# Kernel tuning notes

Hardware: AMD Instinct MI355X
Metric: run time of the kernel (lower is better)

The kernel has to match this reference:

```python
import jax, jax.numpy as jnp
import numpy as np

EMBED_DIM = 1024
NUM_HEADS = 16
HEAD_DIM = EMBED_DIM // NUM_HEADS


def setup_inputs() -> dict:
    key = jax.random.key(0)
    ks = jax.random.split(key, 6)
    s = 1.0 / np.sqrt(EMBED_DIM)
    x = jax.random.normal(ks[0], (2, 2048, EMBED_DIM), dtype=jnp.float32)
    # torch Linear weights are [out, in]; y = x @ W.T
    Wq = jax.random.uniform(ks[1], (EMBED_DIM, EMBED_DIM), jnp.float32, -s, s)
    Wk = jax.random.uniform(ks[2], (EMBED_DIM, EMBED_DIM), jnp.float32, -s, s)
    Wv = jax.random.uniform(ks[3], (EMBED_DIM, EMBED_DIM), jnp.float32, -s, s)
    Wo = jax.random.uniform(ks[4], (EMBED_DIM, EMBED_DIM), jnp.float32, -s, s)
    bo = jax.random.uniform(ks[5], (EMBED_DIM,), jnp.float32, -s, s)
    return {"x": x, "Wq": Wq, "Wk": Wk, "Wv": Wv, "Wo": Wo, "bo": bo}


def reference(x, Wq, Wk, Wv, Wo, bo):
    B, T, C = x.shape
    H, D = NUM_HEADS, HEAD_DIM
    # projections (torch Linear: x @ W.T)
    Q = (x @ Wq.T).reshape(B, T, H, D).transpose(0, 2, 1, 3)  # [B,H,T,D]
    K = (x @ Wk.T).reshape(B, T, H, D).transpose(0, 2, 1, 3)
    V = (x @ Wv.T).reshape(B, T, H, D).transpose(0, 2, 1, 3)
    scores = jnp.einsum('bhqd,bhkd->bhqk', Q, K) / jnp.sqrt(jnp.float32(D))
    causal = jnp.tril(jnp.ones((T, T), dtype=bool))
    scores = jnp.where(causal, scores, -jnp.inf)
    weights = jax.nn.softmax(scores, axis=-1)  # dropout=0.0 (eval): identity
    out = jnp.einsum('bhqk,bhkd->bhqd', weights, V)
    out = out.transpose(0, 2, 1, 3).reshape(B, T, C)
    return out @ Wo.T + bo
```

## Files before the change

### kernel.cpp

```cpp
#include <hip/hip_runtime.h>
#include <stdint.h>

typedef unsigned short u16;
typedef __bf16 bf16x4 __attribute__((ext_vector_type(4)));
typedef __bf16 bf16x8 __attribute__((ext_vector_type(8)));
typedef float f32x4 __attribute__((ext_vector_type(4)));

#define EMBED 1024
#define NHEAD 16
#define HDIM  64
#define BATCH 2
#define SEQ   2048
#define MROWS 4096

__device__ __forceinline__ u16 f2bf(float f) {
  union { float f; uint32_t u; } v; v.f = f;
  uint32_t u = v.u;
  return (u16)((u + 0x7FFFu + ((u >> 16) & 1u)) >> 16);
}

__device__ __forceinline__ float exp2_fast(float x) {
  float r; asm("v_exp_f32 %0, %1" : "=v"(r) : "v"(x)); return r;
}

__device__ __forceinline__ void gload16(const void* g, void* l) {
  __builtin_amdgcn_global_load_lds(
      (__attribute__((address_space(1))) uint32_t*)g,
      (__attribute__((address_space(3))) uint32_t*)l, 16, 0, 0);
}

__global__ __launch_bounds__(256) void convert_all(
    const float* __restrict__ x,  const float* __restrict__ wq,
    const float* __restrict__ wk, const float* __restrict__ wv,
    const float* __restrict__ wo,
    u16* __restrict__ xb, u16* __restrict__ wqb, u16* __restrict__ wkb,
    u16* __restrict__ wvb, u16* __restrict__ wob)
{
  int i4 = (blockIdx.x * 256 + threadIdx.x) * 4;
  const float* src; u16* dst; int off;
  if      (i4 < 4194304) { src = x;  dst = xb;  off = i4; }
  else if (i4 < 5242880) { src = wq; dst = wqb; off = i4 - 4194304; }
  else if (i4 < 6291456) { src = wk; dst = wkb; off = i4 - 5242880; }
  else if (i4 < 7340032) { src = wv; dst = wvb; off = i4 - 6291456; }
  else                   { src = wo; dst = wob; off = i4 - 7340032; }
  float4 v = *(const float4*)&src[off];
  ushort4 u;
  u.x = f2bf(v.x); u.y = f2bf(v.y); u.z = f2bf(v.z); u.w = f2bf(v.w);
  *(ushort4*)&dst[off] = u;
}

__global__ __launch_bounds__(256) void gemm_qkv(
    const u16* __restrict__ Ab, const u16* __restrict__ Wq,
    const u16* __restrict__ Wk, const u16* __restrict__ Wv,
    u16* __restrict__ Qb, u16* __restrict__ Kb, u16* __restrict__ Vt)
{
  const int bid = blockIdx.x;
  const int wg = (bid & 7) * 96 + (bid >> 3);
  const int my = wg / 24, nx = wg % 24;
  const int mode = nx >> 3;
  const u16* Bw = (mode == 0) ? Wq : (mode == 1) ? Wk : Wv;
  const int m0 = my * 128, n0 = (nx & 7) * 128;

  __shared__ __align__(16) u16 As[2][128 * 32];
  __shared__ __align__(16) u16 Bs[2][128 * 32];
  const int tid = threadIdx.x;
  const int lane = tid & 63, wid = tid >> 6;
  const int c = lane & 15, g = lane >> 4;
  const int wm = wid >> 1, wn = wid & 1;

  f32x4 acc[4][4] = {};

  auto stage = [&](int buf, int kt) {
#pragma unroll
    for (int i = 0; i < 2; ++i) {
      int ch = tid + i * 256;
      int row = ch >> 2, col8 = (ch & 3) * 8;
      gload16(Ab + (m0 + row) * 1024 + kt * 32 + col8, &As[buf][ch * 8]);
      gload16(Bw + (n0 + row) * 1024 + kt * 32 + col8, &Bs[buf][ch * 8]);
    }
  };

  stage(0, 0);
  __syncthreads();

  for (int kt = 0; kt < 32; ++kt) {
    const int cur = kt & 1;
    if (kt < 31) stage(cur ^ 1, kt + 1);
    bf16x8 af[4], bfr[4];
#pragma unroll
    for (int mi = 0; mi < 4; ++mi)
      af[mi] = *(const bf16x8*)&As[cur][(wm * 64 + mi * 16 + c) * 32 + g * 8];
#pragma unroll
    for (int ni = 0; ni < 4; ++ni)
      bfr[ni] = *(const bf16x8*)&Bs[cur][(wn * 64 + ni * 16 + c) * 32 + g * 8];
#pragma unroll
    for (int mi = 0; mi < 4; ++mi)
#pragma unroll
      for (int ni = 0; ni < 4; ++ni)
        acc[mi][ni] = __builtin_amdgcn_mfma_f32_16x16x32_bf16(
            af[mi], bfr[ni], acc[mi][ni], 0, 0, 0);
    __syncthreads();
  }

  const int gm = m0 + wm * 64;
  const int gn = n0 + wn * 64;
  if (mode < 2) {
    u16* Out = (mode == 0) ? Qb : Kb;
    const float sc = (mode == 0) ? 0.18033688011112042f : 1.0f;
#pragma unroll
    for (int mi = 0; mi < 4; ++mi)
#pragma unroll
      for (int ni = 0; ni < 4; ++ni)
#pragma unroll
        for (int r = 0; r < 4; ++r) {
          int m = gm + mi * 16 + 4 * g + r;
          int n = gn + ni * 16 + c;
          int b = m >> 11, t = m & 2047, h = n >> 6, d = n & 63;
          Out[((b * NHEAD + h) * SEQ + t) * HDIM + d] = f2bf(acc[mi][ni][r] * sc);
        }
  } else {
#pragma unroll
    for (int mi = 0; mi < 4; ++mi)
#pragma unroll
      for (int ni = 0; ni < 4; ++ni) {
        int m = gm + mi * 16 + 4 * g;
        int n = gn + ni * 16 + c;
        int b = m >> 11, t = m & 2047, h = n >> 6, d = n & 63;
        int tl = t & 63;
        int tp = (t & ~63) + (tl >> 5) * 32 + ((tl >> 2) & 3) * 8
                 + ((tl >> 4) & 1) * 4;
        ushort4 pk;
        pk.x = f2bf(acc[mi][ni][0]);
        pk.y = f2bf(acc[mi][ni][1]);
        pk.z = f2bf(acc[mi][ni][2]);
        pk.w = f2bf(acc[mi][ni][3]);
        *(ushort4*)&Vt[((b * NHEAD + h) * HDIM + d) * SEQ + tp] = pk;
      }
  }
}

__global__ __launch_bounds__(256, 4) void attn(
    const u16* __restrict__ Qb, const u16* __restrict__ Kb,
    const u16* __restrict__ Vt, u16* __restrict__ Ob)
{
  const int bid = blockIdx.x;
  const int xcd = bid & 7, d = bid >> 3;
  const int p = d >> 5, s = d & 31;
  const int bh = xcd * 4 + p;
  const int sp = (s + (p >> 1) * 16) & 31;
  const int qt = (p & 1) ? sp : 31 - sp;
  const int b = bh >> 4, h = bh & 15;
  const int q0 = qt * 64;

  __shared__ __align__(16) u16 Ks[2][64 * 64];
  __shared__ __align__(16) u16 Vs[2][64 * 64];

  const int tid = threadIdx.x, lane = tid & 63, w = tid >> 6;
  const int c = lane & 15, g = lane >> 4;

  const u16* Qg = Qb + bh * SEQ * HDIM;
  const u16* Kg = Kb + bh * SEQ * HDIM;
  const u16* Vg = Vt + bh * HDIM * SEQ;

  bf16x8 qf[2];
#pragma unroll
  for (int kk = 0; kk < 2; ++kk)
    qf[kk] = *(const bf16x8*)&Qg[(q0 + w * 16 + c) * HDIM + kk * 32 + g * 8];

  f32x4 o[4] = {};
  float lacc = 0.f;

  auto stage = [&](int buf, int j) {
    const int k0 = j * 64;
#pragma unroll
    for (int i = 0; i < 2; ++i) {
      int ch = tid + i * 256;
      int row = ch >> 3, c8 = ch & 7;
      int sc8 = c8 ^ (row & 7);
      gload16(Kg + (k0 + row) * HDIM + sc8 * 8, &Ks[buf][ch * 8]);
      gload16(Vg + row * SEQ + k0 + sc8 * 8, &Vs[buf][ch * 8]);
    }
  };

  stage(0, 0);
  __syncthreads();

  for (int j = 0; j <= qt; ++j) {
    const int cur = j & 1;
    if (j < qt) stage(cur ^ 1, j + 1);
    const int k0 = j * 64;

    f32x4 st[4] = {};
    __builtin_amdgcn_s_setprio(1);
#pragma unroll
    for (int kk = 0; kk < 2; ++kk)
#pragma unroll
      for (int kvt = 0; kvt < 4; ++kvt) {
        const int R = kvt * 16 + c;
        bf16x8 kf = *(const bf16x8*)
            &Ks[cur][R * 64 + (((kk * 4 + g) ^ (R & 7)) * 8)];
        st[kvt] = __builtin_amdgcn_mfma_f32_16x16x32_bf16(kf, qf[kk], st[kvt], 0, 0, 0);
      }
    __builtin_amdgcn_s_setprio(0);

    if (j == qt) {
      const int qrow = q0 + w * 16 + c;
#pragma unroll
      for (int kvt = 0; kvt < 4; ++kvt)
#pragma unroll
        for (int r = 0; r < 4; ++r) {
          int kv = k0 + kvt * 16 + 4 * g + r;
          st[kvt][r] = (kv <= qrow) ? st[kvt][r] : -1e30f;
        }
    }

    bf16x8 pa[2];
#pragma unroll
    for (int kvt = 0; kvt < 4; ++kvt)
#pragma unroll
      for (int r = 0; r < 4; ++r) {
        float p2 = exp2_fast(st[kvt][r]);
        lacc += p2;
        pa[kvt >> 1][(kvt & 1) * 4 + r] = (__bf16)p2;
      }

    __builtin_amdgcn_s_setprio(1);
#pragma unroll
    for (int kk = 0; kk < 2; ++kk)
#pragma unroll
      for (int ni = 0; ni < 4; ++ni) {
        const int dd = ni * 16 + c;
        bf16x8 vf = *(const bf16x8*)
            &Vs[cur][dd * 64 + (((kk * 4 + g) ^ (dd & 7)) * 8)];
        o[ni] = __builtin_amdgcn_mfma_f32_16x16x32_bf16(pa[kk], vf, o[ni], 0, 0, 0);
      }
    __builtin_amdgcn_s_setprio(0);

    __syncthreads();
  }

  float rs = lacc;
  rs += __shfl_xor(rs, 16);
  rs += __shfl_xor(rs, 32);
  const float inv = 1.0f / rs;
  float lr[4];
#pragma unroll
  for (int r = 0; r < 4; ++r) lr[r] = __shfl(inv, 4 * g + r);
#pragma unroll
  for (int ni = 0; ni < 4; ++ni)
#pragma unroll
    for (int r = 0; r < 4; ++r) {
      int nc = h * HDIM + ni * 16 + c;
      int mr = b * SEQ + q0 + w * 16 + 4 * g + r;
      Ob[mr * EMBED + nc] = f2bf(o[ni][r] * lr[r]);
    }
}

__global__ __launch_bounds__(256) void gemm_out(
    const u16* __restrict__ Ab, const u16* __restrict__ Bw,
    const float* __restrict__ bias, float* __restrict__ Out)
{
  const int bid = blockIdx.x;
  const int wg = (bid & 7) * 32 + (bid >> 3);
  const int my = wg >> 3, nx = wg & 7;
  const int m0 = my * 128, n0 = nx * 128;

  __shared__ __align__(16) u16 As[2][128 * 32];
  __shared__ __align__(16) u16 Bs[2][128 * 32];
  const int tid = threadIdx.x;
  const int lane = tid & 63, wid = tid >> 6;
  const int c = lane & 15, g = lane >> 4;
  const int wm = wid >> 1, wn = wid & 1;

  f32x4 acc[4][4] = {};

  auto stage = [&](int buf, int kt) {
#pragma unroll
    for (int i = 0; i < 2; ++i) {
      int ch = tid + i * 256;
      int row = ch >> 2, col8 = (ch & 3) * 8;
      gload16(Ab + (m0 + row) * 1024 + kt * 32 + col8, &As[buf][ch * 8]);
      gload16(Bw + (n0 + row) * 1024 + kt * 32 + col8, &Bs[buf][ch * 8]);
    }
  };

  stage(0, 0);
  __syncthreads();

  for (int kt = 0; kt < 32; ++kt) {
    const int cur = kt & 1;
    if (kt < 31) stage(cur ^ 1, kt + 1);
    bf16x8 af[4], bfr[4];
#pragma unroll
    for (int mi = 0; mi < 4; ++mi)
      af[mi] = *(const bf16x8*)&As[cur][(wm * 64 + mi * 16 + c) * 32 + g * 8];
#pragma unroll
    for (int ni = 0; ni < 4; ++ni)
      bfr[ni] = *(const bf16x8*)&Bs[cur][(wn * 64 + ni * 16 + c) * 32 + g * 8];
#pragma unroll
    for (int mi = 0; mi < 4; ++mi)
#pragma unroll
      for (int ni = 0; ni < 4; ++ni)
        acc[mi][ni] = __builtin_amdgcn_mfma_f32_16x16x32_bf16(
            af[mi], bfr[ni], acc[mi][ni], 0, 0, 0);
    __syncthreads();
  }

  const int gm = m0 + wm * 64;
  const int gn = n0 + wn * 64;
#pragma unroll
  for (int mi = 0; mi < 4; ++mi)
#pragma unroll
    for (int ni = 0; ni < 4; ++ni)
#pragma unroll
      for (int r = 0; r < 4; ++r) {
        int m = gm + mi * 16 + 4 * g + r;
        int n = gn + ni * 16 + c;
        Out[m * 1024 + n] = acc[mi][ni][r] + bias[n];
      }
}

extern "C" void kernel_launch(void* const* d_in, const int* in_sizes, int n_in,
                              void* d_out, int out_size, void* d_ws, size_t ws_size,
                              hipStream_t stream) {
  const float* x  = (const float*)d_in[0];
  const float* Wq = (const float*)d_in[1];
  const float* Wk = (const float*)d_in[2];
  const float* Wv = (const float*)d_in[3];
  const float* Wo = (const float*)d_in[4];
  const float* bo = (const float*)d_in[5];
  char* ws = (char*)d_ws;
  u16* xb  = (u16*)(ws);
  u16* wqb = (u16*)(ws + 8388608);
  u16* wkb = (u16*)(ws + 10485760);
  u16* wvb = (u16*)(ws + 12582912);
  u16* wob = (u16*)(ws + 14680064);
  u16* Qb  = (u16*)(ws + 16777216);
  u16* Kb  = (u16*)(ws + 25165824);
  u16* Vt  = (u16*)(ws + 33554432);
  u16* Ob  = (u16*)(ws + 41943040);

  convert_all<<<8192, 256, 0, stream>>>(x, Wq, Wk, Wv, Wo,
                                        xb, wqb, wkb, wvb, wob);
  gemm_qkv<<<dim3(768), 256, 0, stream>>>(xb, wqb, wkb, wvb, Qb, Kb, Vt);
  attn<<<dim3(1024), 256, 0, stream>>>(Qb, Kb, Vt, Ob);
  gemm_out<<<dim3(256), 256, 0, stream>>>(Ob, wob, bo, (float*)d_out);
}
```

Before: 111.4 us.

## Triple-buffer GEMM LDS staging with a single barrier per k-step

Result: slower. 128.6 us (+15.4%).

```diff
diff --git a/kernel.cpp b/kernel.cpp
--- a/kernel.cpp
+++ b/kernel.cpp
@@ -61,8 +61,8 @@
   const u16* Bw = (mode == 0) ? Wq : (mode == 1) ? Wk : Wv;
   const int m0 = my * 128, n0 = (nx & 7) * 128;
 
-  __shared__ __align__(16) u16 As[2][128 * 32];
-  __shared__ __align__(16) u16 Bs[2][128 * 32];
+  __shared__ __align__(16) u16 As[3][128 * 32];
+  __shared__ __align__(16) u16 Bs[3][128 * 32];
   const int tid = threadIdx.x;
   const int lane = tid & 63, wid = tid >> 6;
   const int c = lane & 15, g = lane >> 4;
@@ -80,27 +80,36 @@
     }
   };
 
-  stage(0, 0);
-  __syncthreads();
-
-  for (int kt = 0; kt < 32; ++kt) {
-    const int cur = kt & 1;
-    if (kt < 31) stage(cur ^ 1, kt + 1);
+  auto compute = [&](int buf) {
     bf16x8 af[4], bfr[4];
 #pragma unroll
     for (int mi = 0; mi < 4; ++mi)
-      af[mi] = *(const bf16x8*)&As[cur][(wm * 64 + mi * 16 + c) * 32 + g * 8];
+      af[mi] = *(const bf16x8*)&As[buf][(wm * 64 + mi * 16 + c) * 32 + g * 8];
 #pragma unroll
     for (int ni = 0; ni < 4; ++ni)
-      bfr[ni] = *(const bf16x8*)&Bs[cur][(wn * 64 + ni * 16 + c) * 32 + g * 8];
+      bfr[ni] = *(const bf16x8*)&Bs[buf][(wn * 64 + ni * 16 + c) * 32 + g * 8];
 #pragma unroll
     for (int mi = 0; mi < 4; ++mi)
 #pragma unroll
       for (int ni = 0; ni < 4; ++ni)
         acc[mi][ni] = __builtin_amdgcn_mfma_f32_16x16x32_bf16(
             af[mi], bfr[ni], acc[mi][ni], 0, 0, 0);
-    __syncthreads();
+  };
+
+  stage(0, 0);
+  stage(1, 1);
+  int cur = 0, nx2 = 2;
+  for (int kt = 0; kt < 31; ++kt) {
+    asm volatile("s_waitcnt vmcnt(4)" ::: "memory");
+    __builtin_amdgcn_s_barrier();
+    if (kt + 2 < 32) stage(nx2, kt + 2);
+    compute(cur);
+    cur = (cur == 2) ? 0 : cur + 1;
+    nx2 = (nx2 == 2) ? 0 : nx2 + 1;
   }
+  asm volatile("s_waitcnt vmcnt(0)" ::: "memory");
+  __builtin_amdgcn_s_barrier();
+  compute(cur);
 
   const int gm = m0 + wm * 64;
   const int gn = n0 + wn * 64;
@@ -265,8 +274,8 @@
   const int my = wg >> 3, nx = wg & 7;
   const int m0 = my * 128, n0 = nx * 128;
 
-  __shared__ __align__(16) u16 As[2][128 * 32];
-  __shared__ __align__(16) u16 Bs[2][128 * 32];
+  __shared__ __align__(16) u16 As[3][128 * 32];
+  __shared__ __align__(16) u16 Bs[3][128 * 32];
   const int tid = threadIdx.x;
   const int lane = tid & 63, wid = tid >> 6;
   const int c = lane & 15, g = lane >> 4;
@@ -284,27 +293,36 @@
     }
   };
 
-  stage(0, 0);
-  __syncthreads();
-
-  for (int kt = 0; kt < 32; ++kt) {
-    const int cur = kt & 1;
-    if (kt < 31) stage(cur ^ 1, kt + 1);
+  auto compute = [&](int buf) {
     bf16x8 af[4], bfr[4];
 #pragma unroll
     for (int mi = 0; mi < 4; ++mi)
-      af[mi] = *(const bf16x8*)&As[cur][(wm * 64 + mi * 16 + c) * 32 + g * 8];
+      af[mi] = *(const bf16x8*)&As[buf][(wm * 64 + mi * 16 + c) * 32 + g * 8];
 #pragma unroll
     for (int ni = 0; ni < 4; ++ni)
-      bfr[ni] = *(const bf16x8*)&Bs[cur][(wn * 64 + ni * 16 + c) * 32 + g * 8];
+      bfr[ni] = *(const bf16x8*)&Bs[buf][(wn * 64 + ni * 16 + c) * 32 + g * 8];
 #pragma unroll
     for (int mi = 0; mi < 4; ++mi)
 #pragma unroll
       for (int ni = 0; ni < 4; ++ni)
         acc[mi][ni] = __builtin_amdgcn_mfma_f32_16x16x32_bf16(
             af[mi], bfr[ni], acc[mi][ni], 0, 0, 0);
-    __syncthreads();
+  };
+
+  stage(0, 0);
+  stage(1, 1);
+  int cur = 0, nx2 = 2;
+  for (int kt = 0; kt < 31; ++kt) {
+    asm volatile("s_waitcnt vmcnt(4)" ::: "memory");
+    __builtin_amdgcn_s_barrier();
+    if (kt + 2 < 32) stage(nx2, kt + 2);
+    compute(cur);
+    cur = (cur == 2) ? 0 : cur + 1;
+    nx2 = (nx2 == 2) ? 0 : nx2 + 1;
   }
+  asm volatile("s_waitcnt vmcnt(0)" ::: "memory");
+  __builtin_amdgcn_s_barrier();
+  compute(cur);
 
   const int gm = m0 + wm * 64;
   const int gn = n0 + wn * 64;
```

## Pair complementary causal query tiles per attention block to balance work and share K/V

Applied to the files above, without the earlier changes.

Result: slower. 113.8 us (+2.1%).

```diff
diff --git a/kernel.cpp b/kernel.cpp
--- a/kernel.cpp
+++ b/kernel.cpp
@@ -139,18 +139,19 @@
   }
 }
 
-__global__ __launch_bounds__(256, 4) void attn(
+__global__ __launch_bounds__(256, 2) void attn(
     const u16* __restrict__ Qb, const u16* __restrict__ Kb,
     const u16* __restrict__ Vt, u16* __restrict__ Ob)
 {
   const int bid = blockIdx.x;
   const int xcd = bid & 7, d = bid >> 3;
-  const int p = d >> 5, s = d & 31;
-  const int bh = xcd * 4 + p;
-  const int sp = (s + (p >> 1) * 16) & 31;
-  const int qt = (p & 1) ? sp : 31 - sp;
+  const int cu = d & 31, half = d >> 5;
+  const int bh = xcd * 4 + (cu >> 3);
+  const int sp = cu & 7;
+  const int s = half ? (15 - sp) : sp;
+  const int qtA = s, qtB = 31 - s;
   const int b = bh >> 4, h = bh & 15;
-  const int q0 = qt * 64;
+  const int q0A = qtA * 64, q0B = qtB * 64;
 
   __shared__ __align__(16) u16 Ks[2][64 * 64];
   __shared__ __align__(16) u16 Vs[2][64 * 64];
@@ -162,13 +163,15 @@
   const u16* Kg = Kb + bh * SEQ * HDIM;
   const u16* Vg = Vt + bh * HDIM * SEQ;
 
-  bf16x8 qf[2];
-#pragma unroll
-  for (int kk = 0; kk < 2; ++kk)
-    qf[kk] = *(const bf16x8*)&Qg[(q0 + w * 16 + c) * HDIM + kk * 32 + g * 8];
-
-  f32x4 o[4] = {};
-  float lacc = 0.f;
+  bf16x8 qfA[2], qfB[2];
+#pragma unroll
+  for (int kk = 0; kk < 2; ++kk) {
+    qfA[kk] = *(const bf16x8*)&Qg[(q0A + w * 16 + c) * HDIM + kk * 32 + g * 8];
+    qfB[kk] = *(const bf16x8*)&Qg[(q0B + w * 16 + c) * HDIM + kk * 32 + g * 8];
+  }
+
+  f32x4 oA[4] = {}, oB[4] = {};
+  float laccA = 0.f, laccB = 0.f;
 
   auto stage = [&](int buf, int j) {
     const int k0 = j * 64;
@@ -185,74 +188,126 @@
   stage(0, 0);
   __syncthreads();
 
-  for (int j = 0; j <= qt; ++j) {
+  for (int j = 0; j <= qtB; ++j) {
     const int cur = j & 1;
-    if (j < qt) stage(cur ^ 1, j + 1);
+    if (j < qtB) stage(cur ^ 1, j + 1);
+    const bool dual = (j <= qtA);
     const int k0 = j * 64;
 
-    f32x4 st[4] = {};
+    f32x4 stA[4] = {}, stB[4] = {};
     __builtin_amdgcn_s_setprio(1);
-#pragma unroll
-    for (int kk = 0; kk < 2; ++kk)
-#pragma unroll
-      for (int kvt = 0; kvt < 4; ++kvt) {
-        const int R = kvt * 16 + c;
-        bf16x8 kf = *(const bf16x8*)
-            &Ks[cur][R * 64 + (((kk * 4 + g) ^ (R & 7)) * 8)];
-        st[kvt] = __builtin_amdgcn_mfma_f32_16x16x32_bf16(kf, qf[kk], st[kvt], 0, 0, 0);
-      }
+    if (dual) {
+#pragma unroll
+      for (int kk = 0; kk < 2; ++kk)
+#pragma unroll
+        for (int kvt = 0; kvt < 4; ++kvt) {
+          const int R = kvt * 16 + c;
+          bf16x8 kf = *(const bf16x8*)
+              &Ks[cur][R * 64 + (((kk * 4 + g) ^ (R & 7)) * 8)];
+          stB[kvt] = __builtin_amdgcn_mfma_f32_16x16x32_bf16(kf, qfB[kk], stB[kvt], 0, 0, 0);
+          stA[kvt] = __builtin_amdgcn_mfma_f32_16x16x32_bf16(kf, qfA[kk], stA[kvt], 0, 0, 0);
+        }
+    } else {
+#pragma unroll
+      for (int kk = 0; kk < 2; ++kk)
+#pragma unroll
+        for (int kvt = 0; kvt < 4; ++kvt) {
+          const int R = kvt * 16 + c;
+          bf16x8 kf = *(const bf16x8*)
+              &Ks[cur][R * 64 + (((kk * 4 + g) ^ (R & 7)) * 8)];
+          stB[kvt] = __builtin_amdgcn_mfma_f32_16x16x32_bf16(kf, qfB[kk], stB[kvt], 0, 0, 0);
+        }
+    }
     __builtin_amdgcn_s_setprio(0);
 
-    if (j == qt) {
-      const int qrow = q0 + w * 16 + c;
+    if (j == qtA) {
+      const int qrow = q0A + w * 16 + c;
 #pragma unroll
       for (int kvt = 0; kvt < 4; ++kvt)
 #pragma unroll
         for (int r = 0; r < 4; ++r) {
           int kv = k0 + kvt * 16 + 4 * g + r;
-          st[kvt][r] = (kv <= qrow) ? st[kvt][r] : -1e30f;
-        }
-    }
-
-    bf16x8 pa[2];
+          stA[kvt][r] = (kv <= qrow) ? stA[kvt][r] : -1e30f;
+        }
+    }
+    if (j == qtB) {
+      const int qrow = q0B + w * 16 + c;
+#pragma unroll
+      for (int kvt = 0; kvt < 4; ++kvt)
+#pragma unroll
+        for (int r = 0; r < 4; ++r) {
+          int kv = k0 + kvt * 16 + 4 * g + r;
+          stB[kvt][r] = (kv <= qrow) ? stB[kvt][r] : -1e30f;
+        }
+    }
+
+    bf16x8 paA[2], paB[2];
 #pragma unroll
     for (int kvt = 0; kvt < 4; ++kvt)
 #pragma unroll
       for (int r = 0; r < 4; ++r) {
-        float p2 = exp2_fast(st[kvt][r]);
-        lacc += p2;
-        pa[kvt >> 1][(kvt & 1) * 4 + r] = (__bf16)p2;
+        float pB = exp2_fast(stB[kvt][r]);
+        laccB += pB;
+        paB[kvt >> 1][(kvt & 1) * 4 + r] = (__bf16)pB;
       }
+    if (dual) {
+#pragma unroll
+      for (int kvt = 0; kvt < 4; ++kvt)
+#pragma unroll
+        for (int r = 0; r < 4; ++r) {
+          float pA = exp2_fast(stA[kvt][r]);
+          laccA += pA;
+          paA[kvt >> 1][(kvt & 1) * 4 + r] = (__bf16)pA;
+        }
+    }
 
     __builtin_amdgcn_s_setprio(1);
-#pragma unroll
-    for (int kk = 0; kk < 2; ++kk)
-#pragma unroll
-      for (int ni = 0; ni < 4; ++ni) {
-        const int dd = ni * 16 + c;
-        bf16x8 vf = *(const bf16x8*)
-            &Vs[cur][dd * 64 + (((kk * 4 + g) ^ (dd & 7)) * 8)];
-        o[ni] = __builtin_amdgcn_mfma_f32_16x16x32_bf16(pa[kk], vf, o[ni], 0, 0, 0);
-      }
+    if (dual) {
+#pragma unroll
+      for (int kk = 0; kk < 2; ++kk)
+#pragma unroll
+        for (int ni = 0; ni < 4; ++ni) {
+          const int dd = ni * 16 + c;
+          bf16x8 vf = *(const bf16x8*)
+              &Vs[cur][dd * 64 + (((kk * 4 + g) ^ (dd & 7)) * 8)];
+          oB[ni] = __builtin_amdgcn_mfma_f32_16x16x32_bf16(paB[kk], vf, oB[ni], 0, 0, 0);
+          oA[ni] = __builtin_amdgcn_mfma_f32_16x16x32_bf16(paA[kk], vf, oA[ni], 0, 0, 0);
+        }
+    } else {
+#pragma unroll
+      for (int kk = 0; kk < 2; ++kk)
+#pragma unroll
+        for (int ni = 0; ni < 4; ++ni) {
+          const int dd = ni * 16 + c;
+          bf16x8 vf = *(const bf16x8*)
+              &Vs[cur][dd * 64 + (((kk * 4 + g) ^ (dd & 7)) * 8)];
+          oB[ni] = __builtin_amdgcn_mfma_f32_16x16x32_bf16(paB[kk], vf, oB[ni], 0, 0, 0);
+        }
+    }
     __builtin_amdgcn_s_setprio(0);
 
     __syncthreads();
   }
 
-  float rs = lacc;
-  rs += __shfl_xor(rs, 16);
-  rs += __shfl_xor(rs, 32);
-  const float inv = 1.0f / rs;
-  float lr[4];
-#pragma unroll
-  for (int r = 0; r < 4; ++r) lr[r] = __shfl(inv, 4 * g + r);
+  float rsA = laccA, rsB = laccB;
+  rsA += __shfl_xor(rsA, 16); rsA += __shfl_xor(rsA, 32);
+  rsB += __shfl_xor(rsB, 16); rsB += __shfl_xor(rsB, 32);
+  const float invA = 1.0f / rsA, invB = 1.0f / rsB;
+  float lrA[4], lrB[4];
+#pragma unroll
+  for (int r = 0; r < 4; ++r) {
+    lrA[r] = __shfl(invA, 4 * g + r);
+    lrB[r] = __shfl(invB, 4 * g + r);
+  }
 #pragma unroll
   for (int ni = 0; ni < 4; ++ni)
 #pragma unroll
     for (int r = 0; r < 4; ++r) {
       int nc = h * HDIM + ni * 16 + c;
-      int mr = b * SEQ + q0 + w * 16 + 4 * g + r;
-      Ob[mr * EMBED + nc] = f2bf(o[ni][r] * lr[r]);
+      int mrA = b * SEQ + q0A + w * 16 + 4 * g + r;
+      Ob[mrA * EMBED + nc] = f2bf(oA[ni][r] * lrA[r]);
+      int mrB = b * SEQ + q0B + w * 16 + 4 * g + r;
+      Ob[mrB * EMBED + nc] = f2bf(oB[ni][r] * lrB[r]);
     }
 }
 
@@ -343,6 +398,6 @@
   convert_all<<<8192, 256, 0, stream>>>(x, Wq, Wk, Wv, Wo,
                                         xb, wqb, wkb, wvb, wob);
   gemm_qkv<<<dim3(768), 256, 0, stream>>>(xb, wqb, wkb, wvb, Qb, Kb, Vt);
-  attn<<<dim3(1024), 256, 0, stream>>>(Qb, Kb, Vt, Ob);
+  attn<<<dim3(512), 256, 0, stream>>>(Qb, Kb, Vt, Ob);
   gemm_out<<<dim3(256), 256, 0, stream>>>(Ob, wob, bo, (float*)d_out);
 }
```
